# Kernel tuning notes

Measured on AMD Instinct MI355X. Metric: run time of the kernel, lower is better.

Reference implementation:

```python
import jax, jax.numpy as jnp
import numpy as np

N, E, G = 20000, 640000, 64
D_IN, H, C, D_OUT = 256, 4, 64, 32
HC = H * C


def gat_layer(x, W, a_src, a_dst, b, src, dst, n_nodes, heads, ch):
    # x: [N, F_in], W: [F_in, H*C]
    h = (x @ W).reshape(n_nodes, heads, ch)          # [N,H,C]
    es = jnp.einsum('nhc,hc->nh', h, a_src)          # [N,H]
    ed = jnp.einsum('nhc,hc->nh', h, a_dst)
    e = jax.nn.leaky_relu(es[src] + ed[dst], 0.2)    # [Etot,H]
    m = jax.ops.segment_max(e, dst, num_segments=n_nodes)
    m = jnp.where(jnp.isfinite(m), m, 0.0)
    ex = jnp.exp(e - m[dst])
    denom = jax.ops.segment_sum(ex, dst, num_segments=n_nodes)
    alpha = ex / jnp.maximum(denom[dst], 1e-16)      # softmax over in-edges per dst
    out = jax.ops.segment_sum(alpha[:, :, None] * h[src], dst, num_segments=n_nodes)
    return out.reshape(n_nodes, heads * ch) + b


def setup_inputs() -> dict:
    key = jax.random.key(0)
    ks = jax.random.split(key, 14)
    g1 = 1.0 / np.sqrt(D_IN)
    g2 = 1.0 / np.sqrt(HC)
    inp = {
        'x': jax.random.normal(ks[0], (N, D_IN), jnp.float32),
        'edge_index': jax.random.randint(ks[1], (2, E), 0, N, jnp.int64 if jax.config.jax_enable_x64 else jnp.int32),
        'batch': jnp.sort(jax.random.randint(ks[2], (N,), 0, G)),
        'W1': jax.random.normal(ks[3], (D_IN, HC), jnp.float32) * g1,
        'a_src1': jax.random.normal(ks[4], (H, C), jnp.float32) * g2,
        'a_dst1': jax.random.normal(ks[5], (H, C), jnp.float32) * g2,
        'b1': jnp.zeros((HC,), jnp.float32),
        'W2': jax.random.normal(ks[6], (HC, HC), jnp.float32) * g2,
        'a_src2': jax.random.normal(ks[7], (H, C), jnp.float32) * g2,
        'a_dst2': jax.random.normal(ks[8], (H, C), jnp.float32) * g2,
        'b2': jnp.zeros((HC,), jnp.float32),
        'Wp': jax.random.normal(ks[9], (HC, D_OUT), jnp.float32) * g2,
        'bp': jnp.zeros((D_OUT,), jnp.float32),
    }
    return inp


def reference(x, edge_index, batch, W1, a_src1, a_dst1, b1, W2, a_src2, a_dst2, b2, Wp, bp):
    # add self-loops (PyG GATConv default)
    loop = jnp.arange(N, dtype=edge_index.dtype)
    src = jnp.concatenate([edge_index[0], loop])
    dst = jnp.concatenate([edge_index[1], loop])
    x1 = jax.nn.relu(gat_layer(x, W1, a_src1, a_dst1, b1, src, dst, N, H, C))
    # dropout p=0.6 is identity in eval mode
    x2 = jax.nn.relu(gat_layer(x1, W2, a_src2, a_dst2, b2, src, dst, N, H, C))
    node_scores = x2 @ Wp + bp                        # [N, D_OUT]
    sums = jax.ops.segment_sum(node_scores, batch, num_segments=G)
    counts = jax.ops.segment_sum(jnp.ones((N,), node_scores.dtype), batch, num_segments=G)
    return sums / jnp.maximum(counts, 1.0)[:, None]   # [G, D_OUT]
```

## Files before the change

kernel.cpp:

```cpp
#include <hip/hip_runtime.h>
#include <hip/hip_bf16.h>
#include <cstdint>

#define NNODES 20000
#define NEDGES 640000
#define ETOT   (NEDGES + NNODES)
#define NGROUP 64
#define HC     256
#define DOUT   32

typedef short bf16x8 __attribute__((ext_vector_type(8)));
typedef short s16x4  __attribute__((ext_vector_type(4)));
typedef float f32x4  __attribute__((ext_vector_type(4)));

__device__ __forceinline__ float b2f(__hip_bfloat16 v) { return __bfloat162float(v); }
__device__ __forceinline__ float bs2f(short v) {
    union { unsigned int u; float f; } c; c.u = ((unsigned int)(unsigned short)v) << 16; return c.f;
}
__device__ __forceinline__ short f2bs(float v) {
    __hip_bfloat16 b = __float2bfloat16(v);
    union { __hip_bfloat16 b; short s; } u; u.b = b; return u.s;
}
__device__ __forceinline__ float ldf(const void* __restrict__ p, size_t i, int bf) {
    return bf ? __bfloat162float(((const __hip_bfloat16*)p)[i]) : ((const float*)p)[i];
}
__device__ __forceinline__ int ld_idx(const int* __restrict__ p, size_t i, int f64) {
    return f64 ? p[2 * i] : p[i];
}

__global__ void k_probe(const unsigned int* __restrict__ xw, const int* __restrict__ ei,
                        int* __restrict__ flag, int* __restrict__ deg) {
    int t = blockIdx.x * 256 + threadIdx.x;
    for (int i = t; i < NNODES; i += 256 * 32) deg[i] = 0;
    if (blockIdx.x == 0 && threadIdx.x < 64) {
        int l = threadIdx.x;
        int ones = 0, zeros = 0;
#pragma unroll
        for (int r = 0; r < 4; r++) {
            unsigned long long b1 = __ballot((xw[r * 64 + l] >> 14) & 1);
            unsigned long long b2 = __ballot(ei[2 * (r * 64 + l) + 1] == 0);
            ones  += __popcll(b1);
            zeros += __popcll(b2);
        }
        if (l == 0) { flag[1] = (ones < 64) ? 1 : 0; flag[0] = (zeros > 200) ? 1 : 0; }
    }
}

__global__ void k_hist(const int* __restrict__ ei, int* __restrict__ deg,
                       const int* __restrict__ flag) {
    int i = blockIdx.x * blockDim.x + threadIdx.x;
    if (i >= ETOT) return;
    int f = flag[0];
    int d = (i < NEDGES) ? ld_idx(ei, (size_t)NEDGES + i, f) : (i - NEDGES);
    atomicAdd(&deg[d], 1);
}

__global__ void k_scan(const int* __restrict__ deg, int* __restrict__ off, int* __restrict__ cur,
                       float* __restrict__ sx, int* __restrict__ cnt) {
    __shared__ int wsum[8];
    int t = threadIdx.x, lane = t & 63, wv = t >> 6;
    for (int i = t; i < NGROUP * HC; i += 512) sx[i] = 0.f;
    if (t < NGROUP) cnt[t] = 0;
    const int CH = ((NNODES + 511) / 512) * 64;
    int base = wv * CH;
    int s = 0;
    for (int i0 = 0; i0 < CH; i0 += 64) {
        int i = base + i0 + lane;
        s += (i < NNODES) ? deg[i] : 0;
    }
#pragma unroll
    for (int o = 1; o < 64; o <<= 1) s += __shfl_xor(s, o);
    if (lane == 0) wsum[wv] = s;
    __syncthreads();
    int run = 0;
    for (int i = 0; i < wv; i++) run += wsum[i];
    for (int i0 = 0; i0 < CH; i0 += 64) {
        int i = base + i0 + lane;
        int v = (i < NNODES) ? deg[i] : 0;
        int sc = v;
#pragma unroll
        for (int o = 1; o < 64; o <<= 1) {
            int u = __shfl_up(sc, o);
            if (lane >= o) sc += u;
        }
        if (i < NNODES) { int ex = run + sc - v; off[i] = ex; cur[i] = ex; }
        run += __shfl(sc, 63);
    }
    if (t == 0) off[NNODES] = ETOT;
}

__global__ void k_scatter(const int* __restrict__ ei, int* __restrict__ cur,
                          int* __restrict__ csr, const int* __restrict__ flag) {
    int i = blockIdx.x * blockDim.x + threadIdx.x;
    if (i >= ETOT) return;
    int f = flag[0];
    int s, d;
    if (i < NEDGES) { s = ld_idx(ei, i, f); d = ld_idx(ei, (size_t)NEDGES + i, f); }
    else            { s = d = i - NEDGES; }
    int pos = atomicAdd(&cur[d], 1);
    csr[pos] = s;
}

__global__ void k_wt(const void* __restrict__ W1, const void* __restrict__ W2,
                     __hip_bfloat16* __restrict__ Wt1, __hip_bfloat16* __restrict__ Wt2,
                     const int* __restrict__ flag) {
    int i = blockIdx.x * 256 + threadIdx.x;
    int which = i >> 16;
    int j = i & 65535;
    int k = j >> 8, n = j & 255;
    const void* W = which ? W2 : W1;
    __hip_bfloat16* Wt = which ? Wt2 : Wt1;
    Wt[(size_t)n * 256 + k] = __float2bfloat16(ldf(W, (size_t)k * 256 + n, flag[1]));
}

__global__ __launch_bounds__(256) void k_gemm(const void* __restrict__ A,
                                              const __hip_bfloat16* __restrict__ Bt,
                                              __hip_bfloat16* __restrict__ Hout,
                                              const void* __restrict__ a_src,
                                              const void* __restrict__ a_dst,
                                              float* __restrict__ es4, float* __restrict__ ed4,
                                              const int* __restrict__ flag, int force_bf) {
    int bf   = flag[1];
    int abf  = force_bf | bf;
    int w    = threadIdx.x >> 6;
    int lane = threadIdx.x & 63;
    int mr   = lane & 15;
    int quad = lane >> 4;
    int r0   = blockIdx.x * 16;
    if (r0 >= NNODES) return;
    f32x4 acc[4];
#pragma unroll
    for (int j = 0; j < 4; j++) acc[j] = (f32x4){0.f, 0.f, 0.f, 0.f};
    size_t rowoff = (size_t)(r0 + mr) * HC;
    const __hip_bfloat16* Btw = Bt + (size_t)w * 64 * HC;
    for (int kk = 0; kk < HC; kk += 32) {
        bf16x8 a;
        if (abf) {
            a = *reinterpret_cast<const bf16x8*>((const __hip_bfloat16*)A + rowoff + kk + quad * 8);
        } else {
            const float* af = (const float*)A + rowoff + kk + quad * 8;
            f32x4 lo = *reinterpret_cast<const f32x4*>(af);
            f32x4 hi = *reinterpret_cast<const f32x4*>(af + 4);
#pragma unroll
            for (int ii = 0; ii < 4; ii++) { a[ii] = f2bs(lo[ii]); a[ii + 4] = f2bs(hi[ii]); }
        }
#pragma unroll
        for (int j = 0; j < 4; j++) {
            bf16x8 b = *reinterpret_cast<const bf16x8*>(Btw + (size_t)(j * 16 + mr) * HC + kk + quad * 8);
            acc[j] = __builtin_amdgcn_mfma_f32_16x16x32_bf16(a, b, acc[j], 0, 0, 0);
        }
    }
#pragma unroll
    for (int j = 0; j < 4; j++)
#pragma unroll
        for (int r = 0; r < 4; r++)
            Hout[(size_t)(r0 + quad * 4 + r) * HC + w * 64 + j * 16 + mr] = __float2bfloat16(acc[j][r]);
    float ps[4] = {0.f, 0.f, 0.f, 0.f}, pd[4] = {0.f, 0.f, 0.f, 0.f};
#pragma unroll
    for (int j = 0; j < 4; j++) {
        float asv = ldf(a_src, (size_t)(w * 64 + j * 16 + mr), bf);
        float adv = ldf(a_dst, (size_t)(w * 64 + j * 16 + mr), bf);
#pragma unroll
        for (int r = 0; r < 4; r++) {
            ps[r] = fmaf(acc[j][r], asv, ps[r]);
            pd[r] = fmaf(acc[j][r], adv, pd[r]);
        }
    }
#pragma unroll
    for (int o = 1; o < 16; o <<= 1)
#pragma unroll
        for (int r = 0; r < 4; r++) {
            ps[r] += __shfl_xor(ps[r], o);
            pd[r] += __shfl_xor(pd[r], o);
        }
    if (mr == 0)
#pragma unroll
        for (int r = 0; r < 4; r++) {
            int row = r0 + quad * 4 + r;
            es4[(size_t)row * 4 + w] = ps[r];
            ed4[(size_t)row * 4 + w] = pd[r];
        }
}

__global__ __launch_bounds__(256) void k_agg(const __hip_bfloat16* __restrict__ Hb,
                                             const float* __restrict__ es4, const float* __restrict__ ed4,
                                             const void* __restrict__ bias,
                                             const int* __restrict__ off, const int* __restrict__ csr,
                                             const int* __restrict__ flag,
                                             __hip_bfloat16* __restrict__ out) {
    __shared__ float p_lds[4][256];
    __shared__ int   s_lds[4][64];
    int wv = threadIdx.x >> 6;
    int l  = threadIdx.x & 63;
    int n  = blockIdx.x * 4 + wv;
    int half = l >> 5;
    int hl   = l & 31;
    int hd8  = hl >> 3;
    int base = off[n], deg = off[n + 1] - base;
    f32x4 edv = *reinterpret_cast<const f32x4*>(ed4 + (size_t)n * 4);
    f32x4 m    = (f32x4){-INFINITY, -INFINITY, -INFINITY, -INFINITY};
    f32x4 dsum = (f32x4){0.f, 0.f, 0.f, 0.f};
    float acc[8];
#pragma unroll
    for (int k = 0; k < 8; k++) acc[k] = 0.f;
    for (int c0 = 0; c0 < deg; c0 += 64) {
        int cn = min(deg - c0, 64);
        int s = (l < cn) ? csr[base + c0 + l] : 0;
        s_lds[wv][l] = s;
        f32x4 ev;
        if (l < cn) {
            f32x4 e = *reinterpret_cast<const f32x4*>(es4 + (size_t)s * 4);
#pragma unroll
            for (int h = 0; h < 4; h++) {
                float t = e[h] + edv[h];
                ev[h] = (t > 0.f) ? t : 0.2f * t;
            }
        } else {
#pragma unroll
            for (int h = 0; h < 4; h++) ev[h] = -INFINITY;
        }
        f32x4 mc = ev;
#pragma unroll
        for (int o = 32; o; o >>= 1)
#pragma unroll
            for (int h = 0; h < 4; h++) mc[h] = fmaxf(mc[h], __shfl_xor(mc[h], o));
        f32x4 al, pv;
#pragma unroll
        for (int h = 0; h < 4; h++) {
            float nm = fmaxf(m[h], mc[h]);
            al[h] = __expf(m[h] - nm);
            m[h]  = nm;
        }
#pragma unroll
        for (int h = 0; h < 4; h++) pv[h] = (l < cn) ? __expf(ev[h] - m[h]) : 0.f;
        f32x4 sc = pv;
#pragma unroll
        for (int o = 32; o; o >>= 1)
#pragma unroll
            for (int h = 0; h < 4; h++) sc[h] += __shfl_xor(sc[h], o);
#pragma unroll
        for (int h = 0; h < 4; h++) dsum[h] = dsum[h] * al[h] + sc[h];
        float a8 = al[hd8];
#pragma unroll
        for (int k = 0; k < 8; k++) acc[k] *= a8;
        *reinterpret_cast<f32x4*>(&p_lds[wv][l * 4]) = pv;
        int jn = (cn + 15) & ~15;
        for (int j = 0; j < jn; j += 16) {
            bf16x8 hv[8];
            float pj[8];
#pragma unroll
            for (int i = 0; i < 8; i++) {
                int e  = j + 2 * i + half;
                int sj = s_lds[wv][e];
                hv[i] = *reinterpret_cast<const bf16x8*>(Hb + (size_t)sj * HC + hl * 8);
                pj[i] = p_lds[wv][e * 4 + hd8];
            }
#pragma unroll
            for (int i = 0; i < 8; i++)
#pragma unroll
                for (int k = 0; k < 8; k++) acc[k] = fmaf(pj[i], bs2f(hv[i][k]), acc[k]);
        }
    }
#pragma unroll
    for (int k = 0; k < 8; k++) acc[k] += __shfl_xor(acc[k], 32);
    float dd = fmaxf(dsum[hd8], 1e-16f);
    float rin = 1.0f / dd;
    int bf = flag[1];
    if (half == 0) {
        bf16x8 ov;
#pragma unroll
        for (int k = 0; k < 8; k++) {
            float v = acc[k] * rin + ldf(bias, (size_t)hl * 8 + k, bf);
            ov[k] = f2bs(fmaxf(v, 0.f));
        }
        *reinterpret_cast<bf16x8*>(out + (size_t)n * HC + hl * 8) = ov;
    }
}

__global__ __launch_bounds__(256) void k_groupsum(const __hip_bfloat16* __restrict__ X2,
                                                  const int* __restrict__ batch,
                                                  float* __restrict__ sx, int* __restrict__ cnt,
                                                  const int* __restrict__ flag) {
    const int RPB = NNODES / 250;
    int b = blockIdx.x, f = flag[0];
    int sub = threadIdx.x >> 6, l = threadIdx.x & 63;
    int r = b * RPB + sub;
    f32x4 acc = (f32x4){0.f, 0.f, 0.f, 0.f};
    int curg = ld_idx(batch, r, f);
    int cacc = 0;
    for (int k = 0; k < RPB / 4; k++, r += 4) {
        int g = ld_idx(batch, r, f);
        if (g != curg) {
#pragma unroll
            for (int c = 0; c < 4; c++) atomicAdd(&sx[(size_t)curg * HC + l * 4 + c], acc[c]);
            if (l == 0) atomicAdd(&cnt[curg], cacc);
            acc = (f32x4){0.f, 0.f, 0.f, 0.f}; cacc = 0; curg = g;
        }
        s16x4 hv = *reinterpret_cast<const s16x4*>(X2 + (size_t)r * HC + l * 4);
#pragma unroll
        for (int c = 0; c < 4; c++) acc[c] += bs2f(hv[c]);
        cacc++;
    }
#pragma unroll
    for (int c = 0; c < 4; c++) atomicAdd(&sx[(size_t)curg * HC + l * 4 + c], acc[c]);
    if (l == 0) atomicAdd(&cnt[curg], cacc);
}

__global__ __launch_bounds__(256) void k_final(const float* __restrict__ sx,
                                               const void* __restrict__ Wp,
                                               const void* __restrict__ bp,
                                               const int* __restrict__ cnt,
                                               const int* __restrict__ flag,
                                               void* __restrict__ out) {
    __shared__ float red[8][32];
    int g = blockIdx.x, t = threadIdx.x;
    int c = t & 31, seg = t >> 5;
    int bf = flag[1];
    const float* sxg = sx + (size_t)g * HC;
    float a = 0.f;
#pragma unroll
    for (int k = 0; k < 32; k++) {
        int kk = seg * 32 + k;
        a = fmaf(sxg[kk], ldf(Wp, (size_t)kk * DOUT + c, bf), a);
    }
    red[seg][c] = a;
    __syncthreads();
    if (t < 32) {
        float s = 0.f;
#pragma unroll
        for (int i = 0; i < 8; i++) s += red[i][t];
        int ct = cnt[g];
        float v = (ct > 0) ? (s / ct + ldf(bp, (size_t)t, bf)) : 0.f;
        if (bf) ((__hip_bfloat16*)out)[g * DOUT + t] = __float2bfloat16(v);
        else    ((float*)out)[g * DOUT + t]          = v;
    }
}

extern "C" void kernel_launch(void* const* d_in, const int* in_sizes, int n_in,
                              void* d_out, int out_size, void* d_ws, size_t ws_size,
                              hipStream_t stream) {
    (void)in_sizes; (void)n_in; (void)out_size; (void)ws_size;
    const void* x   = d_in[0];
    const int*  ei  = (const int*)d_in[1];
    const int*  bat = (const int*)d_in[2];
    const void* W1  = d_in[3];
    const void* as1 = d_in[4];
    const void* ad1 = d_in[5];
    const void* b1  = d_in[6];
    const void* W2  = d_in[7];
    const void* as2 = d_in[8];
    const void* ad2 = d_in[9];
    const void* b2  = d_in[10];
    const void* Wp  = d_in[11];
    const void* bp  = d_in[12];

    char* ws = (char*)d_ws;
    size_t o = 0;
    auto alloc = [&](size_t bytes) -> char* {
        char* p = ws + o;
        o += (bytes + 255) & ~(size_t)255;
        return p;
    };
    __hip_bfloat16* hb  = (__hip_bfloat16*)alloc((size_t)NNODES * HC * 2);
    __hip_bfloat16* xb  = (__hip_bfloat16*)alloc((size_t)NNODES * HC * 2);
    __hip_bfloat16* xb2 = (__hip_bfloat16*)alloc((size_t)NNODES * HC * 2);
    __hip_bfloat16* Wt1 = (__hip_bfloat16*)alloc((size_t)HC * HC * 2);
    __hip_bfloat16* Wt2 = (__hip_bfloat16*)alloc((size_t)HC * HC * 2);
    float* es = (float*)alloc((size_t)NNODES * 4 * 4);
    float* ed = (float*)alloc((size_t)NNODES * 4 * 4);
    int* deg  = (int*)alloc((size_t)NNODES * 4);
    int* cur  = (int*)alloc((size_t)NNODES * 4);
    int* off  = (int*)alloc((size_t)(NNODES + 1) * 4);
    int* csr  = (int*)alloc((size_t)ETOT * 4);
    float* sx = (float*)alloc((size_t)NGROUP * HC * 4);
    int* cnt  = (int*)alloc(256);
    int* flag = (int*)alloc(256);

    k_probe<<<32, 256, 0, stream>>>((const unsigned int*)x, ei, flag, deg);
    k_hist<<<(ETOT + 255) / 256, 256, 0, stream>>>(ei, deg, flag);
    k_scan<<<1, 512, 0, stream>>>(deg, off, cur, sx, cnt);
    k_scatter<<<(ETOT + 255) / 256, 256, 0, stream>>>(ei, cur, csr, flag);
    k_wt<<<512, 256, 0, stream>>>(W1, W2, Wt1, Wt2, flag);

    k_gemm<<<NNODES / 16, 256, 0, stream>>>(x, Wt1, hb, as1, ad1, es, ed, flag, 0);
    k_agg<<<NNODES / 4, 256, 0, stream>>>(hb, es, ed, b1, off, csr, flag, xb);

    k_gemm<<<NNODES / 16, 256, 0, stream>>>(xb, Wt2, hb, as2, ad2, es, ed, flag, 1);
    k_agg<<<NNODES / 4, 256, 0, stream>>>(hb, es, ed, b2, off, csr, flag, xb2);

    k_groupsum<<<250, 256, 0, stream>>>(xb2, bat, sx, cnt, flag);
    k_final<<<NGROUP, 256, 0, stream>>>(sx, Wp, bp, cnt, flag, d_out);
}
```

Measured before the change: 351.1 us.

## Split edge softmax into separate score kernel and simplify aggregation loop

Moves the per-destination softmax into a new k_score kernel. It makes two passes over the in-edges (max, then exp and sum), writes unnormalized edge weights to a global alpha buffer, and writes the reciprocal denominator per node. k_agg then only gathers alpha and neighbour features, using vectorized LDS reads, packed bf16-to-float conversion with f32x2 FMAs, and a persistent loop where each wave handles two nodes. This removes the online-softmax rescaling and shuffles from the bandwidth-bound gather loop. In exchange it adds an extra kernel launch per layer and extra global traffic for the alpha buffer (ETOT*16 bytes written and read) plus a second es4 gather.

```diff
diff --git a/kernel.cpp b/kernel.cpp
--- a/kernel.cpp
+++ b/kernel.cpp
@@ -12,6 +12,9 @@
 typedef short bf16x8 __attribute__((ext_vector_type(8)));
 typedef short s16x4  __attribute__((ext_vector_type(4)));
 typedef float f32x4  __attribute__((ext_vector_type(4)));
+typedef float f32x2  __attribute__((ext_vector_type(2)));
+typedef int   s32x4  __attribute__((ext_vector_type(4)));
+typedef unsigned int u32x4 __attribute__((ext_vector_type(4)));
 
 __device__ __forceinline__ float b2f(__hip_bfloat16 v) { return __bfloat162float(v); }
 __device__ __forceinline__ float bs2f(short v) {
@@ -182,98 +185,150 @@
         }
 }
 
+__global__ __launch_bounds__(256) void k_score(const float* __restrict__ es4,
+                                               const float* __restrict__ ed4,
+                                               const int* __restrict__ off, const int* __restrict__ csr,
+                                               float* __restrict__ alpha, float* __restrict__ rinv4) {
+    int wv = threadIdx.x >> 6;
+    int l  = threadIdx.x & 63;
+    int n0 = blockIdx.x * 4 + wv;
+    for (int n = n0; n < NNODES; n += 10000) {
+        int base = off[n], deg = off[n + 1] - base;
+        f32x4 edv = *reinterpret_cast<const f32x4*>(ed4 + (size_t)n * 4);
+        f32x4 m = (f32x4){-INFINITY, -INFINITY, -INFINITY, -INFINITY};
+        for (int c0 = 0; c0 < deg; c0 += 64) {
+            int cn = min(deg - c0, 64);
+            f32x4 ev;
+            if (l < cn) {
+                int s = csr[base + c0 + l];
+                f32x4 e = *reinterpret_cast<const f32x4*>(es4 + (size_t)s * 4);
+#pragma unroll
+                for (int h = 0; h < 4; h++) {
+                    float t = e[h] + edv[h];
+                    ev[h] = (t > 0.f) ? t : 0.2f * t;
+                }
+            } else {
+#pragma unroll
+                for (int h = 0; h < 4; h++) ev[h] = -INFINITY;
+            }
+#pragma unroll
+            for (int o = 32; o; o >>= 1)
+#pragma unroll
+                for (int h = 0; h < 4; h++) ev[h] = fmaxf(ev[h], __shfl_xor(ev[h], o));
+#pragma unroll
+            for (int h = 0; h < 4; h++) m[h] = fmaxf(m[h], ev[h]);
+        }
+        f32x4 ds = (f32x4){0.f, 0.f, 0.f, 0.f};
+        for (int c0 = 0; c0 < deg; c0 += 64) {
+            int cn = min(deg - c0, 64);
+            f32x4 pv;
+            if (l < cn) {
+                int s = csr[base + c0 + l];
+                f32x4 e = *reinterpret_cast<const f32x4*>(es4 + (size_t)s * 4);
+#pragma unroll
+                for (int h = 0; h < 4; h++) {
+                    float t = e[h] + edv[h];
+                    t = (t > 0.f) ? t : 0.2f * t;
+                    pv[h] = __expf(t - m[h]);
+                }
+                *reinterpret_cast<f32x4*>(alpha + (size_t)(base + c0 + l) * 4) = pv;
+            } else {
+#pragma unroll
+                for (int h = 0; h < 4; h++) pv[h] = 0.f;
+            }
+#pragma unroll
+            for (int o = 32; o; o >>= 1)
+#pragma unroll
+                for (int h = 0; h < 4; h++) pv[h] += __shfl_xor(pv[h], o);
+#pragma unroll
+            for (int h = 0; h < 4; h++) ds[h] += pv[h];
+        }
+        if (l == 0) {
+            f32x4 rv;
+#pragma unroll
+            for (int h = 0; h < 4; h++) rv[h] = 1.0f / fmaxf(ds[h], 1e-16f);
+            *reinterpret_cast<f32x4*>(rinv4 + (size_t)n * 4) = rv;
+        }
+    }
+}
+
 __global__ __launch_bounds__(256) void k_agg(const __hip_bfloat16* __restrict__ Hb,
-                                             const float* __restrict__ es4, const float* __restrict__ ed4,
+                                             const float* __restrict__ alpha,
+                                             const float* __restrict__ rinv4,
                                              const void* __restrict__ bias,
                                              const int* __restrict__ off, const int* __restrict__ csr,
                                              const int* __restrict__ flag,
                                              __hip_bfloat16* __restrict__ out) {
-    __shared__ float p_lds[4][256];
+    __shared__ float p_lds[4][4][64];
     __shared__ int   s_lds[4][64];
     int wv = threadIdx.x >> 6;
     int l  = threadIdx.x & 63;
-    int n  = blockIdx.x * 4 + wv;
     int half = l >> 5;
     int hl   = l & 31;
     int hd8  = hl >> 3;
-    int base = off[n], deg = off[n + 1] - base;
-    f32x4 edv = *reinterpret_cast<const f32x4*>(ed4 + (size_t)n * 4);
-    f32x4 m    = (f32x4){-INFINITY, -INFINITY, -INFINITY, -INFINITY};
-    f32x4 dsum = (f32x4){0.f, 0.f, 0.f, 0.f};
-    float acc[8];
-#pragma unroll
-    for (int k = 0; k < 8; k++) acc[k] = 0.f;
-    for (int c0 = 0; c0 < deg; c0 += 64) {
-        int cn = min(deg - c0, 64);
-        int s = (l < cn) ? csr[base + c0 + l] : 0;
-        s_lds[wv][l] = s;
-        f32x4 ev;
-        if (l < cn) {
-            f32x4 e = *reinterpret_cast<const f32x4*>(es4 + (size_t)s * 4);
-#pragma unroll
-            for (int h = 0; h < 4; h++) {
-                float t = e[h] + edv[h];
-                ev[h] = (t > 0.f) ? t : 0.2f * t;
+    int bf = flag[1];
+    int n0 = blockIdx.x * 4 + wv;
+    for (int n = n0; n < NNODES; n += 10000) {
+        int base = off[n], deg = off[n + 1] - base;
+        f32x2 acc2[4];
+#pragma unroll
+        for (int d = 0; d < 4; d++) acc2[d] = (f32x2){0.f, 0.f};
+        for (int c0 = 0; c0 < deg; c0 += 64) {
+            int cn = min(deg - c0, 64);
+            int s = 0;
+            f32x4 a4 = (f32x4){0.f, 0.f, 0.f, 0.f};
+            if (l < cn) {
+                s  = csr[base + c0 + l];
+                a4 = *reinterpret_cast<const f32x4*>(alpha + (size_t)(base + c0 + l) * 4);
             }
-        } else {
-#pragma unroll
-            for (int h = 0; h < 4; h++) ev[h] = -INFINITY;
-        }
-        f32x4 mc = ev;
-#pragma unroll
-        for (int o = 32; o; o >>= 1)
-#pragma unroll
-            for (int h = 0; h < 4; h++) mc[h] = fmaxf(mc[h], __shfl_xor(mc[h], o));
-        f32x4 al, pv;
-#pragma unroll
-        for (int h = 0; h < 4; h++) {
-            float nm = fmaxf(m[h], mc[h]);
-            al[h] = __expf(m[h] - nm);
-            m[h]  = nm;
-        }
-#pragma unroll
-        for (int h = 0; h < 4; h++) pv[h] = (l < cn) ? __expf(ev[h] - m[h]) : 0.f;
-        f32x4 sc = pv;
-#pragma unroll
-        for (int o = 32; o; o >>= 1)
-#pragma unroll
-            for (int h = 0; h < 4; h++) sc[h] += __shfl_xor(sc[h], o);
-#pragma unroll
-        for (int h = 0; h < 4; h++) dsum[h] = dsum[h] * al[h] + sc[h];
-        float a8 = al[hd8];
-#pragma unroll
-        for (int k = 0; k < 8; k++) acc[k] *= a8;
-        *reinterpret_cast<f32x4*>(&p_lds[wv][l * 4]) = pv;
-        int jn = (cn + 15) & ~15;
-        for (int j = 0; j < jn; j += 16) {
-            bf16x8 hv[8];
-            float pj[8];
-#pragma unroll
-            for (int i = 0; i < 8; i++) {
-                int e  = j + 2 * i + half;
-                int sj = s_lds[wv][e];
-                hv[i] = *reinterpret_cast<const bf16x8*>(Hb + (size_t)sj * HC + hl * 8);
-                pj[i] = p_lds[wv][e * 4 + hd8];
+            s_lds[wv][l] = s;
+#pragma unroll
+            for (int h = 0; h < 4; h++) p_lds[wv][h][l] = a4[h];
+            int jn = (cn + 15) & ~15;
+            for (int j = 0; j < jn; j += 16) {
+                int e0 = j + 8 * half;
+                s32x4 sA = *reinterpret_cast<const s32x4*>(&s_lds[wv][e0]);
+                s32x4 sB = *reinterpret_cast<const s32x4*>(&s_lds[wv][e0 + 4]);
+                f32x4 pA = *reinterpret_cast<const f32x4*>(&p_lds[wv][hd8][e0]);
+                f32x4 pB = *reinterpret_cast<const f32x4*>(&p_lds[wv][hd8][e0 + 4]);
+                u32x4 hv[8];
+#pragma unroll
+                for (int i = 0; i < 8; i++) {
+                    int sj = (i < 4) ? sA[i & 3] : sB[i & 3];
+                    hv[i] = *reinterpret_cast<const u32x4*>(Hb + (size_t)sj * HC + hl * 8);
+                }
+#pragma unroll
+                for (int i = 0; i < 8; i++) {
+                    float p = (i < 4) ? pA[i & 3] : pB[i & 3];
+#pragma unroll
+                    for (int d = 0; d < 4; d++) {
+                        unsigned int u = hv[i][d];
+                        f32x2 h2;
+                        h2.x = __uint_as_float(u << 16);
+                        h2.y = __uint_as_float(u & 0xFFFF0000u);
+                        acc2[d] += h2 * p;
+                    }
+                }
             }
-#pragma unroll
-            for (int i = 0; i < 8; i++)
-#pragma unroll
-                for (int k = 0; k < 8; k++) acc[k] = fmaf(pj[i], bs2f(hv[i][k]), acc[k]);
-        }
-    }
-#pragma unroll
-    for (int k = 0; k < 8; k++) acc[k] += __shfl_xor(acc[k], 32);
-    float dd = fmaxf(dsum[hd8], 1e-16f);
-    float rin = 1.0f / dd;
-    int bf = flag[1];
-    if (half == 0) {
-        bf16x8 ov;
-#pragma unroll
-        for (int k = 0; k < 8; k++) {
-            float v = acc[k] * rin + ldf(bias, (size_t)hl * 8 + k, bf);
-            ov[k] = f2bs(fmaxf(v, 0.f));
-        }
-        *reinterpret_cast<bf16x8*>(out + (size_t)n * HC + hl * 8) = ov;
+        }
+#pragma unroll
+        for (int d = 0; d < 4; d++) {
+            acc2[d].x += __shfl_xor(acc2[d].x, 32);
+            acc2[d].y += __shfl_xor(acc2[d].y, 32);
+        }
+        f32x4 rv = *reinterpret_cast<const f32x4*>(rinv4 + (size_t)n * 4);
+        float rinv = rv[hd8];
+        if (half == 0) {
+            bf16x8 ov;
+#pragma unroll
+            for (int d = 0; d < 4; d++) {
+                float v0 = acc2[d].x * rinv + ldf(bias, (size_t)hl * 8 + 2 * d, bf);
+                float v1 = acc2[d].y * rinv + ldf(bias, (size_t)hl * 8 + 2 * d + 1, bf);
+                ov[2 * d]     = f2bs(fmaxf(v0, 0.f));
+                ov[2 * d + 1] = f2bs(fmaxf(v1, 0.f));
+            }
+            *reinterpret_cast<bf16x8*>(out + (size_t)n * HC + hl * 8) = ov;
+        }
     }
 }
 
@@ -368,6 +423,8 @@
     __hip_bfloat16* Wt2 = (__hip_bfloat16*)alloc((size_t)HC * HC * 2);
     float* es = (float*)alloc((size_t)NNODES * 4 * 4);
     float* ed = (float*)alloc((size_t)NNODES * 4 * 4);
+    float* alpha = (float*)alloc((size_t)ETOT * 4 * 4);
+    float* rinv  = (float*)alloc((size_t)NNODES * 4 * 4);
     int* deg  = (int*)alloc((size_t)NNODES * 4);
     int* cur  = (int*)alloc((size_t)NNODES * 4);
     int* off  = (int*)alloc((size_t)(NNODES + 1) * 4);
@@ -383,10 +440,12 @@
     k_wt<<<512, 256, 0, stream>>>(W1, W2, Wt1, Wt2, flag);
 
     k_gemm<<<NNODES / 16, 256, 0, stream>>>(x, Wt1, hb, as1, ad1, es, ed, flag, 0);
-    k_agg<<<NNODES / 4, 256, 0, stream>>>(hb, es, ed, b1, off, csr, flag, xb);
+    k_score<<<2500, 256, 0, stream>>>(es, ed, off, csr, alpha, rinv);
+    k_agg<<<2500, 256, 0, stream>>>(hb, alpha, rinv, b1, off, csr, flag, xb);
 
     k_gemm<<<NNODES / 16, 256, 0, stream>>>(xb, Wt2, hb, as2, ad2, es, ed, flag, 1);
-    k_agg<<<NNODES / 4, 256, 0, stream>>>(hb, es, ed, b2, off, csr, flag, xb2);
+    k_score<<<2500, 256, 0, stream>>>(es, ed, off, csr, alpha, rinv);
+    k_agg<<<2500, 256, 0, stream>>>(hb, alpha, rinv, b2, off, csr, flag, xb2);
 
     k_groupsum<<<250, 256, 0, stream>>>(xb2, bat, sx, cnt, flag);
     k_final<<<NGROUP, 256, 0, stream>>>(sx, Wp, bp, cnt, flag, d_out);
```

Result: slower. 361.9 us (+3.1%).
